# Optimization experiments

Hardware: AMD Instinct MI355X
Metric: run time of the kernel (lower is better)

The kernel has to match this reference:

```python
import jax, jax.numpy as jnp
import numpy as np

N_NODES = 100000
DIM_IN = 128
N_PAIRS = 500000
D2 = 2 * DIM_IN  # concat dim = 256


def setup_inputs() -> dict:
    key = jax.random.key(0)
    k_x, k_idx, k_w1, k_b1, k_w2, k_b2 = jax.random.split(key, 6)
    x = jax.random.normal(k_x, (N_NODES, DIM_IN), dtype=jnp.float32)
    junc_index_pair = jax.random.randint(k_idx, (N_PAIRS, 2), 0, N_NODES, dtype=jnp.int64)
    # MLP: Linear(2d -> 2d) + ReLU, then Linear(2d -> 1), both with bias
    s1 = 1.0 / np.sqrt(D2)
    W1 = jax.random.uniform(k_w1, (D2, D2), minval=-s1, maxval=s1, dtype=jnp.float32)
    b1 = jax.random.uniform(k_b1, (D2,), minval=-s1, maxval=s1, dtype=jnp.float32)
    W2 = jax.random.uniform(k_w2, (D2, 1), minval=-s1, maxval=s1, dtype=jnp.float32)
    b2 = jax.random.uniform(k_b2, (1,), minval=-s1, maxval=s1, dtype=jnp.float32)
    return {"x": x, "junc_index_pair": junc_index_pair,
            "W1": W1, "b1": b1, "W2": W2, "b2": b2}


def reference(x, junc_index_pair, W1, b1, W2, b2):
    # gather both endpoints: [n_pairs, dim_in] each
    node_start = x[junc_index_pair[:, 0]]
    node_end = x[junc_index_pair[:, 1]]
    h = jnp.concatenate((node_start, node_end), axis=1)  # [n_pairs, 2*dim_in]
    h = jax.nn.relu(h @ W1 + b1)                          # [n_pairs, 2*dim_in]
    pred = h @ W2 + b2                                    # [n_pairs, 1]
    return pred.squeeze()                                 # [n_pairs]
```

## Files before the change

kernel.cpp:

```cpp
#include <hip/hip_runtime.h>
#include <hip/hip_bf16.h>
#include <stdint.h>

#define NPAIRS 500000
#define NNODES 100000
#define DIM    128
#define D2     256

typedef __bf16 bf16;
typedef __bf16 bf16x8 __attribute__((ext_vector_type(8)));
typedef __bf16 bf16x4 __attribute__((ext_vector_type(4)));
typedef float  f32x4  __attribute__((ext_vector_type(4)));

__global__ void pack_w1p(const float* __restrict__ W1, bf16* __restrict__ w1p) {
    int t = blockIdx.x * 256 + threadIdx.x;
    int lane = t & 63;
    int kks = (t >> 6) & 3;
    int cg  = t >> 8;
    int l15 = lane & 15, lg = lane >> 4;
    int np = cg * 16 + l15;
    int k0 = kks * 32 + lg * 8;
    const float* src = (np < D2) ? (W1 + (long)k0 * D2 + np)
                                 : (W1 + (long)(k0 + 128) * D2 + (np - D2));
    bf16x8 v;
#pragma unroll
    for (int j = 0; j < 8; ++j) v[j] = (bf16)src[(long)j * D2];
    *(bf16x8*)((char*)w1p + ((long)t << 4)) = v;
}

__launch_bounds__(512, 8)
__global__ void gemm_uv(const float* __restrict__ x,
                        const bf16*  __restrict__ w1p,
                        bf16*        __restrict__ UV) {
    __shared__ char xt[64 * 256];
    __shared__ char hs[64 * 256];
    int tid  = threadIdx.x;
    int wave = tid >> 6, lane = tid & 63;
    int l15 = lane & 15, lg = lane >> 4;
    long nb = (long)blockIdx.x * 64;

#pragma unroll
    for (int it = 0; it < 2; ++it) {
        int task = it * 512 + tid;
        int r = task >> 4, c = task & 15;
        long node = nb + r;
        const float* src = x + (node < NNODES ? node : 0) * DIM + c * 8;
        float4 a = ((const float4*)src)[0];
        float4 b = ((const float4*)src)[1];
        bf16x8 v;
        v[0]=(bf16)a.x; v[1]=(bf16)a.y; v[2]=(bf16)a.z; v[3]=(bf16)a.w;
        v[4]=(bf16)b.x; v[5]=(bf16)b.y; v[6]=(bf16)b.z; v[7]=(bf16)b.w;
        *(bf16x8*)(xt + r * 256 + ((c * 16) ^ ((r & 15) << 4))) = v;
    }
    __syncthreads();

#pragma unroll 1
    for (int p = 0; p < 4; ++p) {
        f32x4 acc[4];
#pragma unroll
        for (int nf = 0; nf < 4; ++nf) acc[nf] = (f32x4){0.f, 0.f, 0.f, 0.f};

        int cg = p * 8 + wave;
#pragma unroll
        for (int kks = 0; kks < 4; ++kks) {
            bf16x8 wf = *(const bf16x8*)((const char*)w1p +
                            (((cg * 4 + kks) * 64 + lane) << 4));
            int kbyte = kks * 64 + lg * 16;
#pragma unroll
            for (int nf = 0; nf < 4; ++nf) {
                int r = nf * 16 + l15;
                bf16x8 xf = *(const bf16x8*)(xt + r * 256 + (kbyte ^ ((r & 15) << 4)));
                acc[nf] = __builtin_amdgcn_mfma_f32_16x16x32_bf16(wf, xf, acc[nf], 0, 0, 0);
            }
        }

#pragma unroll
        for (int nf = 0; nf < 4; ++nf) {
            int row  = nf * 16 + l15;
            int col8 = wave * 32 + lg * 8;
            bf16x4 o;
            o[0] = (bf16)acc[nf][0];
            o[1] = (bf16)acc[nf][1];
            o[2] = (bf16)acc[nf][2];
            o[3] = (bf16)acc[nf][3];
            *(bf16x4*)(hs + row * 256 + (col8 ^ ((row & 15) << 4))) = o;
        }
        __syncthreads();

#pragma unroll
        for (int it = 0; it < 2; ++it) {
            int ci = it * 512 + tid;
            int row = ci >> 4, c = ci & 15;
            bf16x8 v = *(const bf16x8*)(hs + row * 256 + ((c * 16) ^ ((row & 15) << 4)));
            long node = nb + row;
            if (node < NNODES)
                *(bf16x8*)(UV + node * 512 + p * 128 + c * 8) = v;
        }
        __syncthreads();
    }
}

__launch_bounds__(512)
__global__ void pair_pred(const bf16* __restrict__ UV, const int* __restrict__ junc,
                          const float* __restrict__ b1, const float* __restrict__ w2,
                          const float* __restrict__ b2, float* __restrict__ out) {
    int tid = threadIdx.x;
    int lane = tid & 63, half = lane >> 5, l31 = lane & 31;
    long gw = (long)blockIdx.x * 8 + (tid >> 6);
    float b1c[8], w2c[8];
#pragma unroll
    for (int e = 0; e < 8; ++e) {
        int col = l31 * 8 + e;
        b1c[e] = b1[col];
        w2c[e] = w2[col];
    }
    float b2v = b2[0];
    const long HALF = NPAIRS / 2;
    for (long q = gw; q < HALF; q += 8192) {
        long p = 2 * q + half;
        int2 ij = ((const int2*)junc)[p];
        bf16x8 u = *(const bf16x8*)(UV + (long)ij.x * 512 + l31 * 8);
        bf16x8 v = *(const bf16x8*)(UV + (long)ij.y * 512 + 256 + l31 * 8);
        float s = 0.f;
#pragma unroll
        for (int e = 0; e < 8; ++e) {
            float h = (float)u[e] + (float)v[e] + b1c[e];
            s = fmaf(fmaxf(h, 0.f), w2c[e], s);
        }
        s += __shfl_xor(s, 1);
        s += __shfl_xor(s, 2);
        s += __shfl_xor(s, 4);
        s += __shfl_xor(s, 8);
        s += __shfl_xor(s, 16);
        if (l31 == 0) out[p] = s + b2v;
    }
}

__global__ void pack_w1(const float* __restrict__ W1, bf16* __restrict__ w1f) {
    int t = blockIdx.x * 256 + threadIdx.x;
    int lane = t & 63;
    int kk = (t >> 6) & 7;
    int cg = t >> 9;
    int l15 = lane & 15, lg = lane >> 4;
    bf16x8 v;
#pragma unroll
    for (int j = 0; j < 8; ++j)
        v[j] = (bf16)W1[(long)(kk * 32 + lg * 8 + j) * D2 + cg * 16 + l15];
    *(bf16x8*)((char*)w1f + ((long)t << 4)) = v;
}

__launch_bounds__(512, 2)
__global__ void fused_fb(const float* __restrict__ x, const int* __restrict__ junc,
                         const bf16* __restrict__ w1f, const float* __restrict__ b1,
                         const float* __restrict__ w2p, const float* __restrict__ b2,
                         float* __restrict__ out) {
    __shared__ char  atile[128 * 512];
    __shared__ float outp[4][128];
    int tid  = threadIdx.x;
    int wave = tid >> 6, lane = tid & 63;
    int l15 = lane & 15, lg = lane >> 4;
    int wr = wave >> 2, wc = wave & 3;
    long base_p = (long)blockIdx.x * 128;

    float bb[4][4], ww[4][4];
#pragma unroll
    for (int m = 0; m < 4; ++m)
#pragma unroll
        for (int r = 0; r < 4; ++r) {
            int hc = wc * 64 + m * 16 + lg * 4 + r;
            bb[m][r] = b1[hc];
            ww[m][r] = w2p[hc];
        }
#pragma unroll
    for (int it = 0; it < 8; ++it) {
        int task  = it * 512 + tid;
        int nr = task >> 4, chunk = task & 15;
        int r = nr >> 1, side = nr & 1;
        long p = base_p + r;
        int idx = (p < NPAIRS) ? junc[p * 2 + side] : 0;
        const float4* src = (const float4*)(x + (long)idx * DIM + chunk * 8);
        float4 a = src[0], b = src[1];
        bf16x8 v;
        v[0]=(bf16)a.x; v[1]=(bf16)a.y; v[2]=(bf16)a.z; v[3]=(bf16)a.w;
        v[4]=(bf16)b.x; v[5]=(bf16)b.y; v[6]=(bf16)b.z; v[7]=(bf16)b.w;
        int bir = side * 256 + chunk * 16;
        *(bf16x8*)(atile + r * 512 + (bir ^ ((r & 31) << 4))) = v;
    }
    __syncthreads();

    f32x4 acc[4][4];
#pragma unroll
    for (int m = 0; m < 4; ++m)
#pragma unroll
        for (int n = 0; n < 4; ++n)
            acc[m][n] = (f32x4){0.f, 0.f, 0.f, 0.f};
#pragma unroll
    for (int kk = 0; kk < 8; ++kk) {
        bf16x8 xf[4];
        int kbyte = kk * 64 + lg * 16;
#pragma unroll
        for (int n = 0; n < 4; ++n) {
            int r = wr * 64 + n * 16 + l15;
            xf[n] = *(const bf16x8*)(atile + r * 512 + (kbyte ^ ((r & 31) << 4)));
        }
#pragma unroll
        for (int m = 0; m < 4; ++m) {
            bf16x8 wf = *(const bf16x8*)((const char*)w1f +
                            ((((wc * 4 + m) * 8 + kk) * 64 + lane) << 4));
#pragma unroll
            for (int n = 0; n < 4; ++n)
                acc[m][n] = __builtin_amdgcn_mfma_f32_16x16x32_bf16(wf, xf[n], acc[m][n], 0, 0, 0);
        }
    }
#pragma unroll
    for (int n = 0; n < 4; ++n) {
        float s = 0.f;
#pragma unroll
        for (int m = 0; m < 4; ++m)
#pragma unroll
            for (int r = 0; r < 4; ++r)
                s = fmaf(fmaxf(acc[m][n][r] + bb[m][r], 0.f), ww[m][r], s);
        s += __shfl_xor(s, 16);
        s += __shfl_xor(s, 32);
        if (lg == 0) outp[wc][wr * 64 + n * 16 + l15] = s;
    }
    __syncthreads();
    if (tid < 128) {
        long p = base_p + tid;
        if (p < NPAIRS)
            out[p] = b2[0] + outp[0][tid] + outp[1][tid] + outp[2][tid] + outp[3][tid];
    }
}

extern "C" void kernel_launch(void* const* d_in, const int* in_sizes, int n_in,
                              void* d_out, int out_size, void* d_ws, size_t ws_size,
                              hipStream_t stream) {
    const float* x    = (const float*)d_in[0];
    const int*   junc = (const int*)  d_in[1];
    const float* W1   = (const float*)d_in[2];
    const float* b1   = (const float*)d_in[3];
    const float* W2   = (const float*)d_in[4];
    const float* b2   = (const float*)d_in[5];
    float* out = (float*)d_out;

    const size_t UV_B  = (size_t)NNODES * 512 * 2;
    const size_t NEED  = UV_B + 131072;

    if (ws_size >= NEED) {
        bf16* UV  = (bf16*)d_ws;
        bf16* w1p = (bf16*)((char*)d_ws + UV_B);
        hipLaunchKernelGGL(pack_w1p, dim3(32), dim3(256), 0, stream, W1, w1p);
        hipLaunchKernelGGL(gemm_uv, dim3((NNODES + 63) / 64), dim3(512), 0, stream,
                           x, w1p, UV);
        hipLaunchKernelGGL(pair_pred, dim3(1024), dim3(512), 0, stream,
                           UV, junc, b1, W2, b2, out);
    } else {
        bf16* w1f = (bf16*)d_ws;
        hipLaunchKernelGGL(pack_w1, dim3(32), dim3(256), 0, stream, W1, w1f);
        hipLaunchKernelGGL(fused_fb, dim3((NPAIRS + 127) / 128), dim3(512), 0, stream,
                           x, junc, w1f, b1, W2, b2, out);
    }
}
```

Measured before the change: 107.6 us.

## Counting-sort pairs by first endpoint before the gather-based pair prediction

```diff
diff --git a/kernel.cpp b/kernel.cpp
--- a/kernel.cpp
+++ b/kernel.cpp
@@ -6,11 +6,14 @@
 #define NNODES 100000
 #define DIM    128
 #define D2     256
+#define NNPAD  100352
+#define SCANB  98
 
 typedef __bf16 bf16;
 typedef __bf16 bf16x8 __attribute__((ext_vector_type(8)));
 typedef __bf16 bf16x4 __attribute__((ext_vector_type(4)));
 typedef float  f32x4  __attribute__((ext_vector_type(4)));
+typedef unsigned long long u64;
 
 __global__ void pack_w1p(const float* __restrict__ W1, bf16* __restrict__ w1p) {
     int t = blockIdx.x * 256 + threadIdx.x;
@@ -97,6 +100,91 @@
                 *(bf16x8*)(UV + node * 512 + p * 128 + c * 8) = v;
         }
         __syncthreads();
+    }
+}
+
+__global__ void zero_cnt(int* __restrict__ cnt) {
+    cnt[blockIdx.x * 1024 + threadIdx.x] = 0;
+}
+
+__global__ void hist_i(const int* __restrict__ junc, int* __restrict__ cnt) {
+    int p = blockIdx.x * 512 + threadIdx.x;
+    if (p < NPAIRS) atomicAdd(&cnt[((const int2*)junc)[p].x], 1);
+}
+
+__global__ void scan_blk(const int* __restrict__ cnt, int* __restrict__ off,
+                         int* __restrict__ bsum) {
+    __shared__ int s[1024];
+    int t = threadIdx.x, g = blockIdx.x * 1024 + t;
+    int v = cnt[g];
+    s[t] = v;
+    __syncthreads();
+    for (int d = 1; d < 1024; d <<= 1) {
+        int add = (t >= d) ? s[t - d] : 0;
+        __syncthreads();
+        s[t] += add;
+        __syncthreads();
+    }
+    off[g] = s[t] - v;
+    if (t == 1023) bsum[blockIdx.x] = s[t];
+}
+
+__global__ void scan_top(const int* __restrict__ bsum, int* __restrict__ boff) {
+    if (threadIdx.x == 0) {
+        int run = 0;
+        for (int b = 0; b < SCANB; ++b) { boff[b] = run; run += bsum[b]; }
+    }
+}
+
+__global__ void scatter_pairs(const int* __restrict__ junc, int* __restrict__ off,
+                              const int* __restrict__ boff, u64* __restrict__ sorted) {
+    int p = blockIdx.x * 512 + threadIdx.x;
+    if (p >= NPAIRS) return;
+    int2 ij = ((const int2*)junc)[p];
+    int pos = boff[ij.x >> 10] + atomicAdd(&off[ij.x], 1);
+    sorted[pos] = (u64)ij.x | ((u64)ij.y << 17) | ((u64)p << 34);
+}
+
+__launch_bounds__(512)
+__global__ void pair_pred_sorted(const bf16* __restrict__ UV,
+                                 const u64* __restrict__ sorted,
+                                 const float* __restrict__ b1,
+                                 const float* __restrict__ w2,
+                                 const float* __restrict__ b2,
+                                 float* __restrict__ out) {
+    int tid = threadIdx.x;
+    int lane = tid & 63, half = lane >> 5, l31 = lane & 31;
+    long w = (long)blockIdx.x * 8 + (tid >> 6);
+    const long RPW = (NPAIRS + 8191) / 8192;
+    long start = w * RPW;
+    long end = start + RPW; if (end > NPAIRS) end = NPAIRS;
+    float b1c[8], w2c[8];
+#pragma unroll
+    for (int e = 0; e < 8; ++e) {
+        int col = l31 * 8 + e;
+        b1c[e] = b1[col];
+        w2c[e] = w2[col];
+    }
+    float b2v = b2[0];
+    for (long k = start + half; k < end; k += 2) {
+        u64 rec = sorted[k];
+        int i = (int)(rec & 131071u);
+        int j = (int)((rec >> 17) & 131071u);
+        int p = (int)(rec >> 34);
+        bf16x8 u = *(const bf16x8*)(UV + (long)i * 512 + l31 * 8);
+        bf16x8 v = *(const bf16x8*)(UV + (long)j * 512 + 256 + l31 * 8);
+        float s = 0.f;
+#pragma unroll
+        for (int e = 0; e < 8; ++e) {
+            float h = (float)u[e] + (float)v[e] + b1c[e];
+            s = fmaf(fmaxf(h, 0.f), w2c[e], s);
+        }
+        s += __shfl_xor(s, 1);
+        s += __shfl_xor(s, 2);
+        s += __shfl_xor(s, 4);
+        s += __shfl_xor(s, 8);
+        s += __shfl_xor(s, 16);
+        if (l31 == 0) out[p] = s + b2v;
     }
 }
 
@@ -243,15 +331,40 @@
     const float* b2   = (const float*)d_in[5];
     float* out = (float*)d_out;
 
-    const size_t UV_B  = (size_t)NNODES * 512 * 2;
-    const size_t NEED  = UV_B + 131072;
-
-    if (ws_size >= NEED) {
+    const size_t UV_B   = (size_t)NNODES * 512 * 2;
+    const size_t W1P_B  = 131072;
+    const size_t SORT_B = (size_t)NPAIRS * 8;
+    const size_t CNT_B  = (size_t)NNPAD * 4;
+    const size_t OFF_B  = (size_t)NNPAD * 4;
+    const size_t BS_B   = 512, BO_B = 512;
+    const size_t NEED_SORT  = UV_B + W1P_B + SORT_B + CNT_B + OFF_B + BS_B + BO_B;
+    const size_t NEED_BASIC = UV_B + W1P_B;
+
+    if (ws_size >= NEED_SORT) {
+        char* base = (char*)d_ws;
+        bf16* UV     = (bf16*)base;
+        bf16* w1p    = (bf16*)(base + UV_B);
+        u64*  sorted = (u64*) (base + UV_B + W1P_B);
+        int*  cnt    = (int*) (base + UV_B + W1P_B + SORT_B);
+        int*  off    = (int*) (base + UV_B + W1P_B + SORT_B + CNT_B);
+        int*  bsum   = (int*) (base + UV_B + W1P_B + SORT_B + CNT_B + OFF_B);
+        int*  boff   = (int*) (base + UV_B + W1P_B + SORT_B + CNT_B + OFF_B + BS_B);
+
+        hipLaunchKernelGGL(pack_w1p, dim3(32), dim3(256), 0, stream, W1, w1p);
+        hipLaunchKernelGGL(zero_cnt, dim3(SCANB), dim3(1024), 0, stream, cnt);
+        hipLaunchKernelGGL(hist_i, dim3((NPAIRS + 511) / 512), dim3(512), 0, stream, junc, cnt);
+        hipLaunchKernelGGL(scan_blk, dim3(SCANB), dim3(1024), 0, stream, cnt, off, bsum);
+        hipLaunchKernelGGL(scan_top, dim3(1), dim3(64), 0, stream, bsum, boff);
+        hipLaunchKernelGGL(scatter_pairs, dim3((NPAIRS + 511) / 512), dim3(512), 0, stream,
+                           junc, off, boff, sorted);
+        hipLaunchKernelGGL(gemm_uv, dim3((NNODES + 63) / 64), dim3(512), 0, stream, x, w1p, UV);
+        hipLaunchKernelGGL(pair_pred_sorted, dim3(1024), dim3(512), 0, stream,
+                           UV, sorted, b1, W2, b2, out);
+    } else if (ws_size >= NEED_BASIC) {
         bf16* UV  = (bf16*)d_ws;
         bf16* w1p = (bf16*)((char*)d_ws + UV_B);
         hipLaunchKernelGGL(pack_w1p, dim3(32), dim3(256), 0, stream, W1, w1p);
-        hipLaunchKernelGGL(gemm_uv, dim3((NNODES + 63) / 64), dim3(512), 0, stream,
-                           x, w1p, UV);
+        hipLaunchKernelGGL(gemm_uv, dim3((NNODES + 63) / 64), dim3(512), 0, stream, x, w1p, UV);
         hipLaunchKernelGGL(pair_pred, dim3(1024), dim3(512), 0, stream,
                            UV, junc, b1, W2, b2, out);
     } else {
```

After: 145.0 us. 34.7% more time.

## Quantize per-node U/V projections to int8 with per-row scales

Applied to the files above, without the earlier changes.

```diff
diff --git a/kernel.cpp b/kernel.cpp
--- a/kernel.cpp
+++ b/kernel.cpp
@@ -28,12 +28,14 @@
     *(bf16x8*)((char*)w1p + ((long)t << 4)) = v;
 }
 
-__launch_bounds__(512, 8)
-__global__ void gemm_uv(const float* __restrict__ x,
-                        const bf16*  __restrict__ w1p,
-                        bf16*        __restrict__ UV) {
+__launch_bounds__(512, 6)
+__global__ void gemm_uv8(const float* __restrict__ x,
+                         const bf16*  __restrict__ w1p,
+                         int8_t*      __restrict__ UV8,
+                         float*       __restrict__ Su,
+                         float*       __restrict__ Sv) {
     __shared__ char xt[64 * 256];
-    __shared__ char hs[64 * 256];
+    __shared__ char hs[64 * 512];
     int tid  = threadIdx.x;
     int wave = tid >> 6, lane = tid & 63;
     int l15 = lane & 15, lg = lane >> 4;
@@ -55,55 +57,77 @@
     __syncthreads();
 
 #pragma unroll 1
-    for (int p = 0; p < 4; ++p) {
-        f32x4 acc[4];
-#pragma unroll
-        for (int nf = 0; nf < 4; ++nf) acc[nf] = (f32x4){0.f, 0.f, 0.f, 0.f};
-
-        int cg = p * 8 + wave;
-#pragma unroll
-        for (int kks = 0; kks < 4; ++kks) {
-            bf16x8 wf = *(const bf16x8*)((const char*)w1p +
-                            (((cg * 4 + kks) * 64 + lane) << 4));
-            int kbyte = kks * 64 + lg * 16;
+    for (int half = 0; half < 2; ++half) {
+#pragma unroll 1
+        for (int pp = 0; pp < 2; ++pp) {
+            f32x4 acc[4];
+#pragma unroll
+            for (int nf = 0; nf < 4; ++nf) acc[nf] = (f32x4){0.f, 0.f, 0.f, 0.f};
+
+            int cg = (half * 2 + pp) * 8 + wave;
+#pragma unroll
+            for (int kks = 0; kks < 4; ++kks) {
+                bf16x8 wf = *(const bf16x8*)((const char*)w1p +
+                                (((cg * 4 + kks) * 64 + lane) << 4));
+                int kbyte = kks * 64 + lg * 16;
+#pragma unroll
+                for (int nf = 0; nf < 4; ++nf) {
+                    int r = nf * 16 + l15;
+                    bf16x8 xf = *(const bf16x8*)(xt + r * 256 + (kbyte ^ ((r & 15) << 4)));
+                    acc[nf] = __builtin_amdgcn_mfma_f32_16x16x32_bf16(wf, xf, acc[nf], 0, 0, 0);
+                }
+            }
 #pragma unroll
             for (int nf = 0; nf < 4; ++nf) {
-                int r = nf * 16 + l15;
-                bf16x8 xf = *(const bf16x8*)(xt + r * 256 + (kbyte ^ ((r & 15) << 4)));
-                acc[nf] = __builtin_amdgcn_mfma_f32_16x16x32_bf16(wf, xf, acc[nf], 0, 0, 0);
+                int row  = nf * 16 + l15;
+                int col8 = pp * 256 + wave * 32 + lg * 8;
+                bf16x4 o;
+                o[0] = (bf16)acc[nf][0];
+                o[1] = (bf16)acc[nf][1];
+                o[2] = (bf16)acc[nf][2];
+                o[3] = (bf16)acc[nf][3];
+                *(bf16x4*)(hs + row * 512 + (col8 ^ ((row & 31) << 4))) = o;
             }
         }
-
-#pragma unroll
-        for (int nf = 0; nf < 4; ++nf) {
-            int row  = nf * 16 + l15;
-            int col8 = wave * 32 + lg * 8;
-            bf16x4 o;
-            o[0] = (bf16)acc[nf][0];
-            o[1] = (bf16)acc[nf][1];
-            o[2] = (bf16)acc[nf][2];
-            o[3] = (bf16)acc[nf][3];
-            *(bf16x4*)(hs + row * 256 + (col8 ^ ((row & 15) << 4))) = o;
-        }
         __syncthreads();
 
 #pragma unroll
-        for (int it = 0; it < 2; ++it) {
-            int ci = it * 512 + tid;
-            int row = ci >> 4, c = ci & 15;
-            bf16x8 v = *(const bf16x8*)(hs + row * 256 + ((c * 16) ^ ((row & 15) << 4)));
+        for (int it = 0; it < 8; ++it) {
+            int row = it * 8 + wave;
+            int c = lane * 8;
+            bf16x4 hv = *(const bf16x4*)(hs + row * 512 + (c ^ ((row & 31) << 4)));
+            float f0 = (float)hv[0], f1 = (float)hv[1], f2 = (float)hv[2], f3 = (float)hv[3];
+            float m = fmaxf(fmaxf(fabsf(f0), fabsf(f1)), fmaxf(fabsf(f2), fabsf(f3)));
+            m = fmaxf(m, __shfl_xor(m, 1));
+            m = fmaxf(m, __shfl_xor(m, 2));
+            m = fmaxf(m, __shfl_xor(m, 4));
+            m = fmaxf(m, __shfl_xor(m, 8));
+            m = fmaxf(m, __shfl_xor(m, 16));
+            m = fmaxf(m, __shfl_xor(m, 32));
+            float scale = m * (1.0f / 127.0f);
+            float rs = (m > 1e-20f) ? 127.0f / m : 0.f;
+            int q0 = (int)__builtin_rintf(f0 * rs);
+            int q1 = (int)__builtin_rintf(f1 * rs);
+            int q2 = (int)__builtin_rintf(f2 * rs);
+            int q3 = (int)__builtin_rintf(f3 * rs);
+            uint32_t packed = (uint32_t)(q0 & 255) | ((uint32_t)(q1 & 255) << 8)
+                            | ((uint32_t)(q2 & 255) << 16) | ((uint32_t)(q3 & 255) << 24);
             long node = nb + row;
-            if (node < NNODES)
-                *(bf16x8*)(UV + node * 512 + p * 128 + c * 8) = v;
+            if (node < NNODES) {
+                *(uint32_t*)((char*)UV8 + node * 512 + half * 256 + lane * 4) = packed;
+                if (lane == 0) (half ? Sv : Su)[node] = scale;
+            }
         }
         __syncthreads();
     }
 }
 
 __launch_bounds__(512)
-__global__ void pair_pred(const bf16* __restrict__ UV, const int* __restrict__ junc,
-                          const float* __restrict__ b1, const float* __restrict__ w2,
-                          const float* __restrict__ b2, float* __restrict__ out) {
+__global__ void pair_pred8(const int8_t* __restrict__ UV8,
+                           const float* __restrict__ Su, const float* __restrict__ Sv,
+                           const int* __restrict__ junc,
+                           const float* __restrict__ b1, const float* __restrict__ w2,
+                           const float* __restrict__ b2, float* __restrict__ out) {
     int tid = threadIdx.x;
     int lane = tid & 63, half = lane >> 5, l31 = lane & 31;
     long gw = (long)blockIdx.x * 8 + (tid >> 6);
@@ -119,12 +143,19 @@
     for (long q = gw; q < HALF; q += 8192) {
         long p = 2 * q + half;
         int2 ij = ((const int2*)junc)[p];
-        bf16x8 u = *(const bf16x8*)(UV + (long)ij.x * 512 + l31 * 8);
-        bf16x8 v = *(const bf16x8*)(UV + (long)ij.y * 512 + 256 + l31 * 8);
+        uint2 ur = *(const uint2*)(UV8 + (long)ij.x * 512 + l31 * 8);
+        uint2 vr = *(const uint2*)(UV8 + (long)ij.y * 512 + 256 + l31 * 8);
+        float su = Su[ij.x];
+        float sv = Sv[ij.y];
         float s = 0.f;
 #pragma unroll
         for (int e = 0; e < 8; ++e) {
-            float h = (float)u[e] + (float)v[e] + b1c[e];
+            int du = (e < 4) ? (int)ur.x : (int)ur.y;
+            int dv = (e < 4) ? (int)vr.x : (int)vr.y;
+            int sh = 24 - 8 * (e & 3);
+            int ub = (du << sh) >> 24;
+            int vb = (dv << sh) >> 24;
+            float h = fmaf(su, (float)ub, fmaf(sv, (float)vb, b1c[e]));
             s = fmaf(fmaxf(h, 0.f), w2c[e], s);
         }
         s += __shfl_xor(s, 1);
@@ -243,17 +274,21 @@
     const float* b2   = (const float*)d_in[5];
     float* out = (float*)d_out;
 
-    const size_t UV_B  = (size_t)NNODES * 512 * 2;
-    const size_t NEED  = UV_B + 131072;
+    const size_t UV8_B = (size_t)NNODES * 512;
+    const size_t SU_B  = (size_t)NNODES * 4;
+    const size_t NEED  = UV8_B + 2 * SU_B + 131072;
 
     if (ws_size >= NEED) {
-        bf16* UV  = (bf16*)d_ws;
-        bf16* w1p = (bf16*)((char*)d_ws + UV_B);
+        char* base = (char*)d_ws;
+        int8_t* UV8 = (int8_t*)base;
+        float*  Su  = (float*)(base + UV8_B);
+        float*  Sv  = (float*)(base + UV8_B + SU_B);
+        bf16*   w1p = (bf16*) (base + UV8_B + 2 * SU_B);
         hipLaunchKernelGGL(pack_w1p, dim3(32), dim3(256), 0, stream, W1, w1p);
-        hipLaunchKernelGGL(gemm_uv, dim3((NNODES + 63) / 64), dim3(512), 0, stream,
-                           x, w1p, UV);
-        hipLaunchKernelGGL(pair_pred, dim3(1024), dim3(512), 0, stream,
-                           UV, junc, b1, W2, b2, out);
+        hipLaunchKernelGGL(gemm_uv8, dim3((NNODES + 63) / 64), dim3(512), 0, stream,
+                           x, w1p, UV8, Su, Sv);
+        hipLaunchKernelGGL(pair_pred8, dim3(1024), dim3(512), 0, stream,
+                           UV8, Su, Sv, junc, b1, W2, b2, out);
     } else {
         bf16* w1f = (bf16*)d_ws;
         hipLaunchKernelGGL(pack_w1, dim3(32), dim3(256), 0, stream, W1, w1f);
```

Measured after the change: 179.9 us. +67.2%, slower.
